# Kernel tuning notes

Measured on AMD Instinct MI355X. Metric: run time of the kernel, lower is better.

## Reference

```python
import jax, jax.numpy as jnp
import numpy as np

B, T, C, H = 16, 512, 1080, 20  # batch, seq, embd, heads; head_dim = C // H = 54

def setup_inputs() -> dict:
    key = jax.random.key(0)
    k1, k2, k3, k4, k5 = jax.random.split(key, 5)
    s = 0.02
    return {
        "x": jax.random.normal(k1, (B, T, C), dtype=jnp.float32),
        "W_attn": jax.random.normal(k2, (C, 3 * C), dtype=jnp.float32) * s,
        "b_attn": jax.random.normal(k3, (3 * C,), dtype=jnp.float32) * s,
        "W_proj": jax.random.normal(k4, (C, C), dtype=jnp.float32) * s,
        "b_proj": jax.random.normal(k5, (C,), dtype=jnp.float32) * s,
    }

def reference(x, W_attn, b_attn, W_proj, b_proj):
    Bb, Tt, Cc = x.shape
    hd = Cc // H
    qkv = jnp.einsum('btc,cd->btd', x, W_attn) + b_attn  # [B,T,3C]
    q, k, v = jnp.split(qkv, 3, axis=2)
    # [B,T,C] -> [B,H,T,hd]
    q = q.reshape(Bb, Tt, H, hd).transpose(0, 2, 1, 3)
    k = k.reshape(Bb, Tt, H, hd).transpose(0, 2, 1, 3)
    v = v.reshape(Bb, Tt, H, hd).transpose(0, 2, 1, 3)
    att = jnp.einsum('bhqd,bhkd->bhqk', q, k) * (1.0 / jnp.sqrt(jnp.float32(hd)))
    causal = jnp.tril(jnp.ones((Tt, Tt), dtype=bool))
    att = jnp.where(causal, att, -jnp.inf)
    att = jax.nn.softmax(att, axis=-1)
    y = jnp.einsum('bhqk,bhkd->bhqd', att, v)  # [B,H,T,hd]
    y = y.transpose(0, 2, 1, 3).reshape(Bb, Tt, Cc)
    return jnp.einsum('btc,cd->btd', y, W_proj) + b_proj
```

## Files before the change

### kernel.cpp

```cpp
#include <hip/hip_runtime.h>
#include <hip/hip_bf16.h>

#define B_   16
#define T_   512
#define C_   1080
#define H_   20
#define HD_  54
#define DP_  64
#define M_   (B_ * T_)
#define KP_  1088
#define NT_  17
#define NQKV_ 3840
#define NPRJ_ 1152
#define NBT_ (B_ * H_ * T_)

typedef short bf16x8 __attribute__((ext_vector_type(8)));
typedef float f32x4  __attribute__((ext_vector_type(4)));
typedef unsigned short u16x8 __attribute__((ext_vector_type(8)));

__device__ __forceinline__ void gload_lds16(const void* g, void* l) {
    __builtin_amdgcn_global_load_lds(
        (const __attribute__((address_space(1))) void*)g,
        (__attribute__((address_space(3))) void*)l,
        16, 0, 0);
}

__device__ __forceinline__ unsigned short f2b(float x) {
    return __builtin_bit_cast(unsigned short, __float2bfloat16(x));
}

__global__ __launch_bounds__(256) void cvt_pad(
    const float* __restrict__ src, __hip_bfloat16* __restrict__ dst)
{
    int idx = blockIdx.x * 256 + threadIdx.x;
    if (idx >= M_ * (KP_ / 4)) return;
    int m = idx / (KP_ / 4), c = idx - m * (KP_ / 4);
    ushort4 o;
    if (c < C_ / 4) {
        float4 v = *reinterpret_cast<const float4*>(src + (size_t)m * C_ + c * 4);
        o.x = f2b(v.x); o.y = f2b(v.y); o.z = f2b(v.z); o.w = f2b(v.w);
    } else {
        o.x = o.y = o.z = o.w = 0;
    }
    *reinterpret_cast<ushort4*>(reinterpret_cast<unsigned short*>(dst) + (size_t)m * KP_ + c * 4) = o;
}

__global__ __launch_bounds__(256) void transpose_wqkv(
    const float* __restrict__ W, __hip_bfloat16* __restrict__ Wt)
{
    __shared__ float tile[32][33];
    int n0 = blockIdx.x * 32, k0 = blockIdx.y * 32;
    int tx = threadIdx.x, ty = threadIdx.y;
    int np = n0 + tx;
    int which = np / 1280;
    int rem = np - which * 1280;
    int h = rem >> 6, d = rem & 63;
    int sn = which * C_ + h * HD_ + d;
    bool valid = d < HD_;
    #pragma unroll
    for (int i = 0; i < 32; i += 8) {
        int k = k0 + ty + i;
        tile[ty + i][tx] = (valid && k < C_) ? W[(size_t)k * (3 * C_) + sn] : 0.f;
    }
    __syncthreads();
    #pragma unroll
    for (int i = 0; i < 32; i += 8) {
        int n = n0 + ty + i, k = k0 + tx;
        Wt[(size_t)n * KP_ + k] = __float2bfloat16(tile[tx][ty + i]);
    }
}

__global__ __launch_bounds__(256) void transpose_w(
    const float* __restrict__ W, __hip_bfloat16* __restrict__ Wt,
    int K, int N, int Kp)
{
    __shared__ float tile[32][33];
    int n0 = blockIdx.x * 32, k0 = blockIdx.y * 32;
    int tx = threadIdx.x, ty = threadIdx.y;
    #pragma unroll
    for (int i = 0; i < 32; i += 8) {
        int k = k0 + ty + i, n = n0 + tx;
        tile[ty + i][tx] = (k < K && n < N) ? W[(size_t)k * N + n] : 0.f;
    }
    __syncthreads();
    #pragma unroll
    for (int i = 0; i < 32; i += 8) {
        int n = n0 + ty + i, k = k0 + tx;
        Wt[(size_t)n * Kp + k] = __float2bfloat16(tile[tx][ty + i]);
    }
}

__global__ __launch_bounds__(256) void build_bias(
    const float* __restrict__ b_attn, float* __restrict__ bp)
{
    int i = blockIdx.x * 256 + threadIdx.x;
    if (i < NQKV_) {
        int which = i / 1280, rem = i - which * 1280;
        int h = rem >> 6, d = rem & 63;
        float v = (d < HD_) ? b_attn[which * C_ + h * HD_ + d] : 0.f;
        if (which == 2 && d == 63) v = 1.0f;
        bp[i] = v;
    }
}

__global__ __launch_bounds__(512, 2) void gemm256(
    const unsigned short* __restrict__ A,
    const unsigned short* __restrict__ Bt,
    const float* __restrict__ bias,
    unsigned short* __restrict__ outQ,
    unsigned short* __restrict__ outK,
    unsigned short* __restrict__ outV)
{
    __shared__ __align__(16) char smem[131072];

    const int tid  = threadIdx.x;
    const int lane = tid & 63;
    const int wv   = tid >> 6;
    const int wr   = wv >> 2;
    const int wc   = wv & 3;
    const int lq   = lane & 15;
    const int lg   = lane >> 4;

    const int id  = blockIdx.y * 15 + blockIdx.x;
    const int xcd = id & 7;
    const int j   = id >> 3;
    const int m0  = (xcd * 4 + (j & 3)) * 256;
    const int n0  = (j >> 2) * 256;

    unsigned gA[2], gB[2];
    const int ld0 = tid * 16, ld1 = tid * 16 + 8192;
    #pragma unroll
    for (int i = 0; i < 2; ++i) {
        int ci = tid + i * 512;
        int r  = ci >> 3;
        int kc = (ci & 7) ^ (r & 7);
        gA[i] = (unsigned)(m0 + r) * KP_ + kc * 8;
        gB[i] = (unsigned)(n0 + r) * KP_ + kc * 8;
    }
    const unsigned HALFSTEP = 128u * KP_;

    auto stage = [&](int buf, int hIdx, unsigned k0) {
        char* sb = smem + buf * 65536 +
                   (hIdx < 2 ? hIdx * 16384 : 32768 + (hIdx - 2) * 16384);
        const unsigned short* sp = (hIdx < 2) ? A : Bt;
        unsigned extra = (hIdx & 1) ? HALFSTEP : 0u;
        gload_lds16(sp + ((hIdx < 2) ? gA[0] : gB[0]) + extra + k0, sb + ld0);
        gload_lds16(sp + ((hIdx < 2) ? gA[1] : gB[1]) + extra + k0, sb + ld1);
    };

    const int s0 = (lg ^ (lq & 7)) * 16;
    const int s1 = ((4 + lg) ^ (lq & 7)) * 16;
    const int aBase = wr * 16384 + lq * 128;
    const int bBase = 32768 + (wc >> 1) * 16384 + (wc & 1) * 8192 + lq * 128;

    f32x4 acc[8][4] = {};

    stage(0, 0, 0); stage(0, 1, 0); stage(0, 2, 0); stage(0, 3, 0);

    for (int t = 0; t < NT_; ++t) {
        const int cur = t & 1;
        if (t + 1 < NT_) {
            const int nb = cur ^ 1;
            const unsigned k0n = (unsigned)(t + 1) * 64;
            stage(nb, 0, k0n); stage(nb, 1, k0n); stage(nb, 2, k0n); stage(nb, 3, k0n);
            asm volatile("s_waitcnt vmcnt(8)" ::: "memory");
        } else {
            asm volatile("s_waitcnt vmcnt(0)" ::: "memory");
        }
        __builtin_amdgcn_s_barrier();

        const char* Ab = smem + cur * 65536 + aBase;
        const char* Bb = smem + cur * 65536 + bBase;

        bf16x8 bfr[4][2];
        #pragma unroll
        for (int ni = 0; ni < 4; ++ni) {
            bfr[ni][0] = *reinterpret_cast<const bf16x8*>(Bb + ni * 2048 + s0);
            bfr[ni][1] = *reinterpret_cast<const bf16x8*>(Bb + ni * 2048 + s1);
        }
        bf16x8 afA[2][2], afB[2][2];
        #pragma unroll
        for (int i = 0; i < 2; ++i) {
            afA[0][i] = *reinterpret_cast<const bf16x8*>(Ab + i * 2048 + s0);
            afA[1][i] = *reinterpret_cast<const bf16x8*>(Ab + i * 2048 + s1);
        }
        __builtin_amdgcn_s_setprio(1);
        #pragma unroll
        for (int q = 0; q < 4; ++q) {
            if (q < 3) {
                #pragma unroll
                for (int i = 0; i < 2; ++i) {
                    if (q & 1) {
                        afA[0][i] = *reinterpret_cast<const bf16x8*>(Ab + ((q + 1) * 2 + i) * 2048 + s0);
                        afA[1][i] = *reinterpret_cast<const bf16x8*>(Ab + ((q + 1) * 2 + i) * 2048 + s1);
                    } else {
                        afB[0][i] = *reinterpret_cast<const bf16x8*>(Ab + ((q + 1) * 2 + i) * 2048 + s0);
                        afB[1][i] = *reinterpret_cast<const bf16x8*>(Ab + ((q + 1) * 2 + i) * 2048 + s1);
                    }
                }
            }
            #pragma unroll
            for (int kk = 0; kk < 2; ++kk)
                #pragma unroll
                for (int i = 0; i < 2; ++i)
                    #pragma unroll
                    for (int ni = 0; ni < 4; ++ni)
                        acc[q * 2 + i][ni] = __builtin_amdgcn_mfma_f32_16x16x32_bf16(
                            (q & 1) ? afB[kk][i] : afA[kk][i], bfr[ni][kk],
                            acc[q * 2 + i][ni], 0, 0, 0);
        }
        __builtin_amdgcn_s_setprio(0);
        __builtin_amdgcn_s_barrier();
    }

    const int which = n0 / 1280;
    if (which < 2) {
        unsigned short* dst = which ? outK : outQ;
        #pragma unroll
        for (int mi = 0; mi < 8; ++mi) {
            int mg = m0 + wr * 128 + mi * 16 + lg * 4;
            int b = mg >> 9, t0 = mg & (T_ - 1);
            #pragma unroll
            for (int ni = 0; ni < 4; ++ni) {
                int nl = wc * 64 + ni * 16 + lq;
                int ng = n0 + nl - which * 1280;
                int h = ng >> 6, d = ng & 63;
                float bs = bias[n0 + nl];
                size_t basei = ((size_t)(b * H_ + h) * T_ + t0) * DP_ + d;
                #pragma unroll
                for (int j2 = 0; j2 < 4; ++j2)
                    dst[basei + (size_t)j2 * DP_] = f2b(acc[mi][ni][j2] + bs);
            }
        }
    } else {
        unsigned short* lt = (unsigned short*)smem;
        #pragma unroll
        for (int hm = 0; hm < 2; ++hm) {
            if (hm == 1) __syncthreads();
            if (wr == hm) {
                #pragma unroll
                for (int mi = 0; mi < 8; ++mi) {
                    int ml = mi * 16 + lg * 4;
                    int mc = ml >> 3, mo = ml & 7;
                    #pragma unroll
                    for (int ni = 0; ni < 4; ++ni) {
                        int nl = wc * 64 + ni * 16 + lq;
                        float bs = bias[n0 + nl];
                        ushort4 pk;
                        pk.x = f2b(acc[mi][ni][0] + bs);
                        pk.y = f2b(acc[mi][ni][1] + bs);
                        pk.z = f2b(acc[mi][ni][2] + bs);
                        pk.w = f2b(acc[mi][ni][3] + bs);
                        int slot = mc ^ ((nl >> 3) & 15);
                        *reinterpret_cast<ushort4*>(lt + nl * 136 + slot * 8 + mo) = pk;
                    }
                }
            }
            __syncthreads();
            #pragma unroll
            for (int it = 0; it < 8; ++it) {
                int idx = it * 512 + tid;
                int c2 = idx >> 4, j2 = idx & 15;
                int slot = j2 ^ ((c2 >> 3) & 15);
                u16x8 v = *reinterpret_cast<const u16x8*>(lt + c2 * 136 + slot * 8);
                int ng = n0 + c2 - 2560;
                int h = ng >> 6, d = ng & 63;
                int mg = m0 + hm * 128 + j2 * 8;
                int b = mg >> 9, t = mg & (T_ - 1);
                *reinterpret_cast<u16x8*>(outV + ((size_t)(b * H_ + h) * DP_ + d) * T_ + t) = v;
            }
        }
    }
}

__global__ __launch_bounds__(256) void gemm_mfma_p(
    const unsigned short* __restrict__ A,
    const unsigned short* __restrict__ Bt,
    const float* __restrict__ bias,
    float* __restrict__ outP)
{
    __shared__ __align__(16) char smem[65536];

    const int tid  = threadIdx.x;
    const int lane = tid & 63;
    const int wv   = tid >> 6;
    const int wm   = (wv >> 1) * 64;
    const int wn   = (wv & 1) * 64;
    const int lr   = lane & 15;
    const int lk   = lane >> 4;

    const int gx  = gridDim.x;
    const int gy  = gridDim.y;
    const int id  = blockIdx.y * gx + blockIdx.x;
    const int xcd = id & 7;
    const int j   = id >> 3;
    const int mpc = gy >> 3;
    const int m0  = (xcd * mpc + j % mpc) * 128;
    const int n0  = (j / mpc) * 128;

    unsigned aOff[4], bOff[4];
    int ciB[4];
    #pragma unroll
    for (int it = 0; it < 4; ++it) {
        int ci = it * 256 + tid;
        int r = ci >> 3, p = ci & 7;
        int kc = p ^ (r & 7);
        aOff[it] = (unsigned)(m0 + r) * KP_ + kc * 8;
        bOff[it] = (unsigned)(n0 + r) * KP_ + kc * 8;
        ciB[it] = ci * 16;
    }
    int aRd[2][4], bRd[2][4];
    #pragma unroll
    for (int kk = 0; kk < 2; ++kk) {
        #pragma unroll
        for (int mi = 0; mi < 4; ++mi) {
            int row = wm + mi * 16 + lr;
            aRd[kk][mi] = row * 128 + ((kk * 4 + lk) ^ (row & 7)) * 16;
            int rowb = wn + mi * 16 + lr;
            bRd[kk][mi] = 16384 + rowb * 128 + ((kk * 4 + lk) ^ (rowb & 7)) * 16;
        }
    }

    f32x4 acc[4][4] = {};

    auto stage = [&](int buf, int kt) {
        const unsigned k0 = kt * 64;
        char* sb = smem + buf * 32768;
        #pragma unroll
        for (int it = 0; it < 4; ++it)
            gload_lds16(A + aOff[it] + k0, sb + ciB[it]);
        #pragma unroll
        for (int it = 0; it < 4; ++it)
            gload_lds16(Bt + bOff[it] + k0, sb + 16384 + ciB[it]);
    };

    stage(0, 0);
    for (int kt = 0; kt < NT_; ++kt) {
        const int c = kt & 1;
        if (kt + 1 < NT_) {
            stage(1 - c, kt + 1);
            asm volatile("s_waitcnt vmcnt(8)" ::: "memory");
        } else {
            asm volatile("s_waitcnt vmcnt(0)" ::: "memory");
        }
        __builtin_amdgcn_s_barrier();
        asm volatile("" ::: "memory");

        const char* base = smem + c * 32768;
        #pragma unroll
        for (int kk = 0; kk < 2; ++kk) {
            bf16x8 af[4], bfr[4];
            #pragma unroll
            for (int mi = 0; mi < 4; ++mi)
                af[mi] = *reinterpret_cast<const bf16x8*>(base + aRd[kk][mi]);
            #pragma unroll
            for (int ni = 0; ni < 4; ++ni)
                bfr[ni] = *reinterpret_cast<const bf16x8*>(base + bRd[kk][ni]);
            #pragma unroll
            for (int mi = 0; mi < 4; ++mi)
                #pragma unroll
                for (int ni = 0; ni < 4; ++ni)
                    acc[mi][ni] = __builtin_amdgcn_mfma_f32_16x16x32_bf16(
                        af[mi], bfr[ni], acc[mi][ni], 0, 0, 0);
        }
        asm volatile("" ::: "memory");
        __builtin_amdgcn_s_barrier();
    }

    #pragma unroll
    for (int mi = 0; mi < 4; ++mi) {
        int mrow = m0 + wm + mi * 16 + lk * 4;
        #pragma unroll
        for (int ni = 0; ni < 4; ++ni) {
            int n = n0 + wn + ni * 16 + lr;
            if (n < C_) {
                float bs = bias[n];
                #pragma unroll
                for (int j2 = 0; j2 < 4; ++j2)
                    outP[(size_t)(mrow + j2) * C_ + n] = acc[mi][ni][j2] + bs;
            }
        }
    }
}

__global__ __launch_bounds__(256) void attn_mfma(
    const unsigned short* __restrict__ Q, const unsigned short* __restrict__ K,
    const unsigned short* __restrict__ Vt, __hip_bfloat16* __restrict__ Y)
{
    __shared__ __align__(16) char kvs[16384];
    __shared__ __align__(16) unsigned short ps[4][16][72];

    const int tid  = threadIdx.x;
    const int lane = tid & 63;
    const int wv   = tid >> 6;
    const int lq   = lane & 15;
    const int lg   = lane >> 4;
    const int bh   = blockIdx.y;
    const int qt   = blockIdx.x;
    const int qbase = qt * 64;
    const float cs = 0.13608276348795434f * 1.44269504f;

    bf16x8 qf[2];
    {
        const unsigned short* qp = Q + ((size_t)bh * T_ + qbase + wv * 16 + lq) * DP_;
        qf[0] = *reinterpret_cast<const bf16x8*>(qp + lg * 8);
        qf[1] = *reinterpret_cast<const bf16x8*>(qp + 32 + lg * 8);
    }

    unsigned kOff[2], vOff[2];
    int ciB[2];
    #pragma unroll
    for (int it = 0; it < 2; ++it) {
        int ci = it * 256 + tid;
        int r = ci >> 3, p = ci & 7;
        int pc = p ^ (r & 7);
        kOff[it] = (unsigned)(r * DP_ + pc * 8);
        vOff[it] = (unsigned)(r * T_ + pc * 8);
        ciB[it] = ci * 16;
    }
    const unsigned short* Kb = K  + (size_t)bh * T_ * DP_;
    const unsigned short* Vb = Vt + (size_t)bh * DP_ * T_;

    f32x4 o[4] = {};
    unsigned short* pbase = &ps[wv][0][0];
    const int nt = qt + 1;

    for (int kt = 0; kt < nt; ++kt) {
        const int kbase = kt * 64;
        #pragma unroll
        for (int it = 0; it < 2; ++it)
            gload_lds16(Kb + kOff[it] + (unsigned)kbase * DP_, kvs + ciB[it]);
        #pragma unroll
        for (int it = 0; it < 2; ++it)
            gload_lds16(Vb + vOff[it] + (unsigned)kbase, kvs + 8192 + ciB[it]);
        __syncthreads();

        f32x4 s[4] = {};
        #pragma unroll
        for (int dc = 0; dc < 2; ++dc) {
            #pragma unroll
            for (int ni = 0; ni < 4; ++ni) {
                int row = ni * 16 + lq;
                int ch  = (dc * 4 + lg) ^ (row & 7);
                bf16x8 kf = *reinterpret_cast<const bf16x8*>(kvs + row * 128 + ch * 16);
                s[ni] = __builtin_amdgcn_mfma_f32_16x16x32_bf16(qf[dc], kf, s[ni], 0, 0, 0);
            }
        }

        if (kt == qt) {
            #pragma unroll
            for (int ni = 0; ni < 4; ++ni) {
                int kg = kbase + ni * 16 + lq;
                #pragma unroll
                for (int j = 0; j < 4; ++j) {
                    int qg = qbase + wv * 16 + lg * 4 + j;
                    s[ni][j] = (kg > qg) ? -3.0e38f : s[ni][j];
                }
            }
        }
        #pragma unroll
        for (int ni = 0; ni < 4; ++ni) {
            #pragma unroll
            for (int j = 0; j < 4; ++j) {
                float p = exp2f(s[ni][j] * cs);
                int qr = lg * 4 + j;
                int cidx = (ni * 2 + (lq >> 3)) ^ (qr & 7);
                pbase[qr * 72 + cidx * 8 + (lq & 7)] = f2b(p);
            }
        }

        asm volatile("s_waitcnt lgkmcnt(0)" ::: "memory");
        __builtin_amdgcn_sched_barrier(0);

        #pragma unroll
        for (int dc = 0; dc < 2; ++dc) {
            int cc = (dc * 4 + lg) ^ (lq & 7);
            bf16x8 pf = *reinterpret_cast<const bf16x8*>(pbase + lq * 72 + cc * 8);
            #pragma unroll
            for (int ni = 0; ni < 4; ++ni) {
                int row = ni * 16 + lq;
                int ch  = (dc * 4 + lg) ^ (row & 7);
                bf16x8 vf = *reinterpret_cast<const bf16x8*>(kvs + 8192 + row * 128 + ch * 16);
                o[ni] = __builtin_amdgcn_mfma_f32_16x16x32_bf16(pf, vf, o[ni], 0, 0, 0);
            }
        }
        __syncthreads();
    }

    const int b = bh / H_, h = bh - b * H_;
    #pragma unroll
    for (int j = 0; j < 4; ++j) {
        float l = __shfl(o[3][j], (lane & 48) | 15, 64);
        float inv = 1.f / l;
        int t = qbase + wv * 16 + lg * 4 + j;
        #pragma unroll
        for (int ni = 0; ni < 4; ++ni) {
            int d = ni * 16 + lq;
            if (d < HD_)
                Y[((size_t)b * T_ + t) * KP_ + h * HD_ + d] =
                    __float2bfloat16(o[ni][j] * inv);
        }
    }
}

extern "C" void kernel_launch(void* const* d_in, const int* in_sizes, int n_in,
                              void* d_out, int out_size, void* d_ws, size_t ws_size,
                              hipStream_t stream)
{
    const float* x      = (const float*)d_in[0];
    const float* W_attn = (const float*)d_in[1];
    const float* b_attn = (const float*)d_in[2];
    const float* W_proj = (const float*)d_in[3];
    const float* b_proj = (const float*)d_in[4];
    float* out = (float*)d_out;

    __hip_bfloat16* xb = (__hip_bfloat16*)d_ws;
    unsigned short* qb = (unsigned short*)(xb + (size_t)M_ * KP_);
    unsigned short* kb = qb + (size_t)NBT_ * DP_;
    unsigned short* vtb = kb + (size_t)NBT_ * DP_;
    __hip_bfloat16* wta = (__hip_bfloat16*)(vtb + (size_t)NBT_ * DP_);
    __hip_bfloat16* wtp = wta + (size_t)NQKV_ * KP_;
    float* bp = (float*)(wtp + (size_t)NPRJ_ * KP_);
    __hip_bfloat16* yb = xb;

    cvt_pad<<<(M_ * (KP_ / 4) + 255) / 256, 256, 0, stream>>>(x, xb);
    transpose_wqkv<<<dim3(NQKV_ / 32, KP_ / 32), dim3(32, 8), 0, stream>>>(W_attn, wta);
    transpose_w<<<dim3(NPRJ_ / 32, KP_ / 32), dim3(32, 8), 0, stream>>>(
        W_proj, wtp, C_, C_, KP_);
    build_bias<<<(NQKV_ + 255) / 256, 256, 0, stream>>>(b_attn, bp);

    gemm256<<<dim3(NQKV_ / 256, M_ / 256), 512, 0, stream>>>(
        (const unsigned short*)xb, (const unsigned short*)wta, bp,
        qb, kb, vtb);

    attn_mfma<<<dim3(T_ / 64, B_ * H_), 256, 0, stream>>>(qb, kb, vtb, yb);

    gemm_mfma_p<<<dim3(NPRJ_ / 128, M_ / 128), 256, 0, stream>>>(
        (const unsigned short*)yb, (const unsigned short*)wtp, b_proj, out);
}
```

Baseline: 186.1 us.

## Fuse fp32-to-bf16 conversion of x into QKV GEMM and merge prep kernels

Removes the separate cvt_pad pass. The QKV GEMM now loads fp32 x directly into registers, converts it to bf16 and writes it into swizzled LDS, while the B operand still goes through global_load_lds. The weight transposes, the bias build and the zeroing of the Y padding columns are merged into one prep launch, with Y now in its own buffer. This trades a full write and re-read of a padded bf16 copy of x, plus three launches, for twice the A-operand bytes per GEMM tile and a register-staged A path that waits on all loads before each barrier.

```diff
diff --git a/kernel.cpp b/kernel.cpp
--- a/kernel.cpp
+++ b/kernel.cpp
@@ -29,82 +29,67 @@
     return __builtin_bit_cast(unsigned short, __float2bfloat16(x));
 }
 
-__global__ __launch_bounds__(256) void cvt_pad(
-    const float* __restrict__ src, __hip_bfloat16* __restrict__ dst)
-{
-    int idx = blockIdx.x * 256 + threadIdx.x;
-    if (idx >= M_ * (KP_ / 4)) return;
-    int m = idx / (KP_ / 4), c = idx - m * (KP_ / 4);
-    ushort4 o;
-    if (c < C_ / 4) {
-        float4 v = *reinterpret_cast<const float4*>(src + (size_t)m * C_ + c * 4);
-        o.x = f2b(v.x); o.y = f2b(v.y); o.z = f2b(v.z); o.w = f2b(v.w);
-    } else {
-        o.x = o.y = o.z = o.w = 0;
-    }
-    *reinterpret_cast<ushort4*>(reinterpret_cast<unsigned short*>(dst) + (size_t)m * KP_ + c * 4) = o;
-}
-
-__global__ __launch_bounds__(256) void transpose_wqkv(
-    const float* __restrict__ W, __hip_bfloat16* __restrict__ Wt)
+__global__ __launch_bounds__(256) void prep(
+    const float* __restrict__ W_attn, const float* __restrict__ W_proj,
+    const float* __restrict__ b_attn,
+    __hip_bfloat16* __restrict__ wta, __hip_bfloat16* __restrict__ wtp,
+    float* __restrict__ bp, __hip_bfloat16* __restrict__ yb)
 {
     __shared__ float tile[32][33];
-    int n0 = blockIdx.x * 32, k0 = blockIdx.y * 32;
-    int tx = threadIdx.x, ty = threadIdx.y;
-    int np = n0 + tx;
-    int which = np / 1280;
-    int rem = np - which * 1280;
-    int h = rem >> 6, d = rem & 63;
-    int sn = which * C_ + h * HD_ + d;
-    bool valid = d < HD_;
-    #pragma unroll
-    for (int i = 0; i < 32; i += 8) {
-        int k = k0 + ty + i;
-        tile[ty + i][tx] = (valid && k < C_) ? W[(size_t)k * (3 * C_) + sn] : 0.f;
-    }
-    __syncthreads();
-    #pragma unroll
-    for (int i = 0; i < 32; i += 8) {
-        int n = n0 + ty + i, k = k0 + tx;
-        Wt[(size_t)n * KP_ + k] = __float2bfloat16(tile[tx][ty + i]);
-    }
-}
-
-__global__ __launch_bounds__(256) void transpose_w(
-    const float* __restrict__ W, __hip_bfloat16* __restrict__ Wt,
-    int K, int N, int Kp)
-{
-    __shared__ float tile[32][33];
-    int n0 = blockIdx.x * 32, k0 = blockIdx.y * 32;
-    int tx = threadIdx.x, ty = threadIdx.y;
-    #pragma unroll
-    for (int i = 0; i < 32; i += 8) {
-        int k = k0 + ty + i, n = n0 + tx;
-        tile[ty + i][tx] = (k < K && n < N) ? W[(size_t)k * N + n] : 0.f;
-    }
-    __syncthreads();
-    #pragma unroll
-    for (int i = 0; i < 32; i += 8) {
-        int n = n0 + ty + i, k = k0 + tx;
-        Wt[(size_t)n * Kp + k] = __float2bfloat16(tile[tx][ty + i]);
-    }
-}
-
-__global__ __launch_bounds__(256) void build_bias(
-    const float* __restrict__ b_attn, float* __restrict__ bp)
-{
-    int i = blockIdx.x * 256 + threadIdx.x;
-    if (i < NQKV_) {
-        int which = i / 1280, rem = i - which * 1280;
+    const int bx = blockIdx.x, by = blockIdx.y;
+    const int tx = threadIdx.x & 31, ty = threadIdx.x >> 5;
+
+    if (bx < 120) {
+        int n0 = bx * 32, k0 = by * 32;
+        int np = n0 + tx;
+        int which = np / 1280;
+        int rem = np - which * 1280;
         int h = rem >> 6, d = rem & 63;
-        float v = (d < HD_) ? b_attn[which * C_ + h * HD_ + d] : 0.f;
-        if (which == 2 && d == 63) v = 1.0f;
-        bp[i] = v;
+        int sn = which * C_ + h * HD_ + d;
+        bool valid = d < HD_;
+        #pragma unroll
+        for (int i = 0; i < 32; i += 8) {
+            int k = k0 + ty + i;
+            tile[ty + i][tx] = (valid && k < C_) ? W_attn[(size_t)k * (3 * C_) + sn] : 0.f;
+        }
+        __syncthreads();
+        #pragma unroll
+        for (int i = 0; i < 32; i += 8) {
+            int n = n0 + ty + i, k = k0 + tx;
+            wta[(size_t)n * KP_ + k] = __float2bfloat16(tile[tx][ty + i]);
+        }
+    } else if (bx < 156) {
+        int n0 = (bx - 120) * 32, k0 = by * 32;
+        #pragma unroll
+        for (int i = 0; i < 32; i += 8) {
+            int k = k0 + ty + i, n = n0 + tx;
+            tile[ty + i][tx] = (k < C_ && n < C_) ? W_proj[(size_t)k * C_ + n] : 0.f;
+        }
+        __syncthreads();
+        #pragma unroll
+        for (int i = 0; i < 32; i += 8) {
+            int n = n0 + ty + i, k = k0 + tx;
+            wtp[(size_t)n * KP_ + k] = __float2bfloat16(tile[tx][ty + i]);
+        }
+    } else if (by == 0) {
+        int seg = bx - 156;
+        if (seg < 15) {
+            int i = seg * 256 + threadIdx.x;
+            int which = i / 1280, rem = i - which * 1280;
+            int h = rem >> 6, d = rem & 63;
+            float v = (d < HD_) ? b_attn[which * C_ + h * HD_ + d] : 0.f;
+            if (which == 2 && d == 63) v = 1.0f;
+            bp[i] = v;
+        } else {
+            int ii = (seg - 15) * 256 + threadIdx.x;
+            int m = ii >> 3, c = ii & 7;
+            yb[(size_t)m * KP_ + C_ + c] = __float2bfloat16(0.f);
+        }
     }
 }
 
 __global__ __launch_bounds__(512, 2) void gemm256(
-    const unsigned short* __restrict__ A,
+    const float* __restrict__ X,
     const unsigned short* __restrict__ Bt,
     const float* __restrict__ bias,
     unsigned short* __restrict__ outQ,
@@ -127,25 +112,62 @@
     const int m0  = (xcd * 4 + (j & 3)) * 256;
     const int n0  = (j >> 2) * 256;
 
-    unsigned gA[2], gB[2];
+    int aDst[4]; unsigned aSrc[4]; int aKc[4];
+    #pragma unroll
+    for (int h = 0; h < 2; ++h)
+        #pragma unroll
+        for (int i = 0; i < 2; ++i) {
+            int cih = tid + i * 512;
+            int r = h * 128 + (cih >> 3);
+            int kc = (cih & 7) ^ (r & 7);
+            int c = h * 2 + i;
+            aDst[c] = h * 16384 + cih * 16;
+            aSrc[c] = (unsigned)(m0 + r) * C_ + kc * 8;
+            aKc[c]  = kc * 8;
+        }
+    unsigned gB[2];
     const int ld0 = tid * 16, ld1 = tid * 16 + 8192;
     #pragma unroll
     for (int i = 0; i < 2; ++i) {
         int ci = tid + i * 512;
-        int r  = ci >> 3;
+        int r = ci >> 3;
         int kc = (ci & 7) ^ (r & 7);
-        gA[i] = (unsigned)(m0 + r) * KP_ + kc * 8;
         gB[i] = (unsigned)(n0 + r) * KP_ + kc * 8;
     }
-    const unsigned HALFSTEP = 128u * KP_;
-
-    auto stage = [&](int buf, int hIdx, unsigned k0) {
-        char* sb = smem + buf * 65536 +
-                   (hIdx < 2 ? hIdx * 16384 : 32768 + (hIdx - 2) * 16384);
-        const unsigned short* sp = (hIdx < 2) ? A : Bt;
-        unsigned extra = (hIdx & 1) ? HALFSTEP : 0u;
-        gload_lds16(sp + ((hIdx < 2) ? gA[0] : gB[0]) + extra + k0, sb + ld0);
-        gload_lds16(sp + ((hIdx < 2) ? gA[1] : gB[1]) + extra + k0, sb + ld1);
+    const unsigned HS = 128u * KP_;
+
+    auto stageB = [&](int buf, unsigned k0) {
+        char* sb = smem + buf * 65536 + 32768;
+        gload_lds16(Bt + gB[0] + k0, sb + ld0);
+        gload_lds16(Bt + gB[1] + k0, sb + ld1);
+        gload_lds16(Bt + gB[0] + HS + k0, sb + 16384 + ld0);
+        gload_lds16(Bt + gB[1] + HS + k0, sb + 16384 + ld1);
+    };
+
+    float4 fv[4][2];
+    auto loadA = [&](unsigned k0) {
+        #pragma unroll
+        for (int c = 0; c < 4; ++c) {
+            const float* p = X + aSrc[c] + k0;
+            fv[c][0] = *reinterpret_cast<const float4*>(p);
+            fv[c][1] = *reinterpret_cast<const float4*>(p + 4);
+        }
+    };
+    auto writeA = [&](int buf, unsigned k0) {
+        char* sb = smem + buf * 65536;
+        #pragma unroll
+        for (int c = 0; c < 4; ++c) {
+            u16x8 o;
+            if (k0 + (unsigned)aKc[c] >= C_) {
+                o = u16x8{0, 0, 0, 0, 0, 0, 0, 0};
+            } else {
+                o[0] = f2b(fv[c][0].x); o[1] = f2b(fv[c][0].y);
+                o[2] = f2b(fv[c][0].z); o[3] = f2b(fv[c][0].w);
+                o[4] = f2b(fv[c][1].x); o[5] = f2b(fv[c][1].y);
+                o[6] = f2b(fv[c][1].z); o[7] = f2b(fv[c][1].w);
+            }
+            *reinterpret_cast<u16x8*>(sb + aDst[c]) = o;
+        }
     };
 
     const int s0 = (lg ^ (lq & 7)) * 16;
@@ -155,19 +177,19 @@
 
     f32x4 acc[8][4] = {};
 
-    stage(0, 0, 0); stage(0, 1, 0); stage(0, 2, 0); stage(0, 3, 0);
+    loadA(0);
+    stageB(0, 0);
+    asm volatile("s_waitcnt vmcnt(4)" ::: "memory");
+    writeA(0, 0);
+    asm volatile("s_waitcnt lgkmcnt(0)" ::: "memory");
+    asm volatile("s_waitcnt vmcnt(0)" ::: "memory");
+    __builtin_amdgcn_s_barrier();
 
     for (int t = 0; t < NT_; ++t) {
-        const int cur = t & 1;
-        if (t + 1 < NT_) {
-            const int nb = cur ^ 1;
-            const unsigned k0n = (unsigned)(t + 1) * 64;
-            stage(nb, 0, k0n); stage(nb, 1, k0n); stage(nb, 2, k0n); stage(nb, 3, k0n);
-            asm volatile("s_waitcnt vmcnt(8)" ::: "memory");
-        } else {
-            asm volatile("s_waitcnt vmcnt(0)" ::: "memory");
-        }
-        __builtin_amdgcn_s_barrier();
+        const int cur = t & 1, nxt = cur ^ 1;
+        const bool pf = (t + 1 < NT_);
+        const unsigned k0n = (unsigned)(t + 1) * 64;
+        if (pf) { loadA(k0n); stageB(nxt, k0n); }
 
         const char* Ab = smem + cur * 65536 + aBase;
         const char* Bb = smem + cur * 65536 + bBase;
@@ -210,6 +232,13 @@
                             acc[q * 2 + i][ni], 0, 0, 0);
         }
         __builtin_amdgcn_s_setprio(0);
+
+        if (pf) {
+            asm volatile("s_waitcnt vmcnt(4)" ::: "memory");
+            writeA(nxt, k0n);
+            asm volatile("s_waitcnt lgkmcnt(0)" ::: "memory");
+            asm volatile("s_waitcnt vmcnt(0)" ::: "memory");
+        }
         __builtin_amdgcn_s_barrier();
     }
 
@@ -514,24 +543,19 @@
     const float* b_proj = (const float*)d_in[4];
     float* out = (float*)d_out;
 
-    __hip_bfloat16* xb = (__hip_bfloat16*)d_ws;
-    unsigned short* qb = (unsigned short*)(xb + (size_t)M_ * KP_);
-    unsigned short* kb = qb + (size_t)NBT_ * DP_;
+    unsigned short* qb  = (unsigned short*)d_ws;
+    unsigned short* kb  = qb + (size_t)NBT_ * DP_;
     unsigned short* vtb = kb + (size_t)NBT_ * DP_;
     __hip_bfloat16* wta = (__hip_bfloat16*)(vtb + (size_t)NBT_ * DP_);
     __hip_bfloat16* wtp = wta + (size_t)NQKV_ * KP_;
     float* bp = (float*)(wtp + (size_t)NPRJ_ * KP_);
-    __hip_bfloat16* yb = xb;
-
-    cvt_pad<<<(M_ * (KP_ / 4) + 255) / 256, 256, 0, stream>>>(x, xb);
-    transpose_wqkv<<<dim3(NQKV_ / 32, KP_ / 32), dim3(32, 8), 0, stream>>>(W_attn, wta);
-    transpose_w<<<dim3(NPRJ_ / 32, KP_ / 32), dim3(32, 8), 0, stream>>>(
-        W_proj, wtp, C_, C_, KP_);
-    build_bias<<<(NQKV_ + 255) / 256, 256, 0, stream>>>(b_attn, bp);
+    __hip_bfloat16* yb = (__hip_bfloat16*)(bp + NQKV_);
+
+    prep<<<dim3(427, 34), 256, 0, stream>>>(W_attn, W_proj, b_attn,
+                                            wta, wtp, bp, yb);
 
     gemm256<<<dim3(NQKV_ / 256, M_ / 256), 512, 0, stream>>>(
-        (const unsigned short*)xb, (const unsigned short*)wta, bp,
-        qb, kb, vtb);
+        x, (const unsigned short*)wta, bp, qb, kb, vtb);
 
     attn_mfma<<<dim3(T_ / 64, B_ * H_), 256, 0, stream>>>(qb, kb, vtb, yb);
 
```

Result: slower. 193.1 us (+3.8%).
